# Performance work log

Measured on AMD Instinct MI355X. Metric: run time of the kernel, lower is better.

The kernel has to match this reference:

```python
import jax, jax.numpy as jnp
import numpy as np


def _conv(x, w, b, pad):
    y = jax.lax.conv_general_dilated(x, w, (1, 1), [(pad, pad), (pad, pad)],
                                     dimension_numbers=('NCHW', 'OIHW', 'NCHW'))
    return y + b[None, :, None, None]


def _pool(x):
    return jax.lax.reduce_window(x, -jnp.inf, jax.lax.max, (1, 1, 2, 2), (1, 1, 2, 2), 'VALID')


def _up(x):
    return jnp.repeat(jnp.repeat(x, 2, axis=2), 2, axis=3)


def _unet(x, p):
    r = jax.nn.relu
    e1 = r(_conv(x, p['enc1_w'], p['enc1_b'], 1))                            # [B,16,H,W]
    e2 = r(_conv(_pool(e1), p['enc2_w'], p['enc2_b'], 1))                    # [B,32,H/2,W/2]
    bt = r(_conv(_pool(e2), p['bott_w'], p['bott_b'], 1))                    # [B,64,H/4,W/4]
    d2 = r(_conv(jnp.concatenate([_up(bt), e2], 1), p['dec2_w'], p['dec2_b'], 1))
    d1 = r(_conv(jnp.concatenate([_up(d2), e1], 1), p['dec1_w'], p['dec1_b'], 1))
    return _conv(d1, p['out_w'], p['out_b'], 0)                              # [B,C,H,W]


def _global_match(ref_e, cur_e):
    # FEELVOS global matching: for each current-frame pixel, distance to the
    # nearest reference-frame pixel in embedding space, mapped through
    # d = 1 - 2/(1+exp(||e_p - e_q||^2)). Monotone, so apply after the min.
    N, E, H, W = ref_e.shape
    a = ref_e.reshape(N, E, H * W).transpose(0, 2, 1)   # [N, P, E] reference pixels
    b = cur_e.reshape(N, E, H * W).transpose(0, 2, 1)   # [N, Q, E] current pixels
    d2 = (jnp.sum(a * a, -1)[:, :, None] + jnp.sum(b * b, -1)[:, None, :]
          - 2.0 * jnp.einsum('npe,nqe->npq', a, b))     # [N, P, Q]
    dmin = jnp.min(jnp.maximum(d2, 0.0), axis=1)        # [N, Q] nearest-neighbor dist^2
    return (1.0 - 2.0 * jax.nn.sigmoid(-dmin)).reshape(N, 1, H, W)


def setup_inputs() -> dict:
    key = jax.random.key(0)
    ks = jax.random.split(key, 16)
    B, C, H, W, CIN = 2, 4, 48, 48, 3

    def w(k, shape):
        fan_in = int(np.prod(shape[1:]))
        return jax.random.normal(k, shape, jnp.float32) * np.float32(1.0 / np.sqrt(fan_in))

    return {
        'x1': jax.random.uniform(ks[0], (B, C, H, W), jnp.float32),
        'x2': jax.random.uniform(ks[1], (B, C, H, W), jnp.float32),
        'x3': jax.random.normal(ks[2], (B, CIN, H, W), jnp.float32),
        'enc1_w': w(ks[3], (16, CIN, 3, 3)), 'enc1_b': jnp.zeros((16,), jnp.float32),
        'enc2_w': w(ks[4], (32, 16, 3, 3)), 'enc2_b': jnp.zeros((32,), jnp.float32),
        'bott_w': w(ks[5], (64, 32, 3, 3)), 'bott_b': jnp.zeros((64,), jnp.float32),
        'dec2_w': w(ks[6], (32, 96, 3, 3)), 'dec2_b': jnp.zeros((32,), jnp.float32),
        'dec1_w': w(ks[7], (16, 48, 3, 3)), 'dec1_b': jnp.zeros((16,), jnp.float32),
        'out_w': w(ks[8], (C, 16, 1, 1)), 'out_b': jnp.zeros((C,), jnp.float32),
        'emb_w': w(ks[9], (100, 1, 3, 3)), 'emb_b': jnp.zeros((100,), jnp.float32),
        'dsh_w': w(ks[10], (1, C + 3, 3, 3)), 'dsh_b': jnp.zeros((1,), jnp.float32),
    }


def reference(x1, x2, x3, enc1_w, enc1_b, enc2_w, enc2_b, bott_w, bott_b,
              dec2_w, dec2_b, dec1_w, dec1_b, out_w, out_b, emb_w, emb_b,
              dsh_w, dsh_b):
    p = dict(enc1_w=enc1_w, enc1_b=enc1_b, enc2_w=enc2_w, enc2_b=enc2_b,
             bott_w=bott_w, bott_b=bott_b, dec2_w=dec2_w, dec2_b=dec2_b,
             dec1_w=dec1_w, dec1_b=dec1_b, out_w=out_w, out_b=out_b)
    B, C, H, W = x1.shape
    x3s = _unet(x3, p)                        # backbone on current frame -> [B,C,H,W]
    # fold the per-class Python loop into the batch axis (shared weights)
    x1f = x1.reshape(B * C, 1, H, W)
    x2f = x2.reshape(B * C, 1, H, W)
    x3f = x3s.reshape(B * C, 1, H, W)
    e1 = _conv(x1f, emb_w, emb_b, 1)          # [B*C,100,H,W]
    e2 = _conv(x2f, emb_w, emb_b, 1)
    e3 = _conv(x3f, emb_w, emb_b, 1)
    gm = _global_match(e1, e3)                # first-frame matching  [B*C,1,H,W]
    lm = _global_match(e2, e3)                # previous-frame matching
    x3rep = jnp.broadcast_to(x3s[:, None], (B, C, C, H, W)).reshape(B * C, C, H, W)
    x_t = jnp.concatenate([x3rep, gm, lm, x2f], axis=1)   # [B*C, C+3, H, W]
    logits = _conv(x_t, dsh_w, dsh_b, 1).reshape(B, C, H, W)
    # faithful to the original final loop: output is cat(logits[C-2], logits[C-1])
    return jnp.concatenate([logits[:, C - 2:C - 1], logits[:, C - 1:C]], axis=1)
```

## Files before the change

kernel.cpp:

```cpp
#include <hip/hip_runtime.h>
#include <math.h>

#define THREADS 256
#define HW 2304

typedef __attribute__((ext_vector_type(8))) short short8;
typedef __attribute__((ext_vector_type(4))) float f32x4;
typedef __attribute__((ext_vector_type(8))) unsigned short us8;

typedef const __attribute__((address_space(1))) void* gas_p;
typedef __attribute__((address_space(3))) void* las_p;

__device__ __forceinline__ void gll16(const void* g, const void* l) {
    __builtin_amdgcn_global_load_lds((gas_p)g, (las_p)l, 16, 0, 0);
}

__device__ __forceinline__ void stage_rows(const float* __restrict__ src, float* __restrict__ dst,
                                           int nch, int chStride, int H, int W,
                                           int rlo, int rcount, int tid, int nthr, bool relu) {
    int rowfl = W + 4;
    int total = nch * rcount * rowfl;
    float4 z = make_float4(0.f, 0.f, 0.f, 0.f);
    for (int i = tid; i * 4 < total; i += nthr) ((float4*)dst)[i] = z;
    __syncthreads();
    int w2 = W >> 1;
    int m = nch * rcount * w2;
    for (int i = tid; i < m; i += nthr) {
        int c2 = i % w2;
        int rr = (i / w2) % rcount;
        int ch = i / (w2 * rcount);
        int srow = rlo + rr;
        if (srow < 0 || srow >= H) continue;
        float2 v = *(const float2*)(src + (size_t)ch * chStride + srow * W + 2 * c2);
        if (relu) { v.x = fmaxf(v.x, 0.f); v.y = fmaxf(v.y, 0.f); }
        *(float2*)(dst + (size_t)ch * rcount * rowfl + rr * rowfl + 2 + 2 * c2) = v;
    }
    __syncthreads();
}

#define LOAD_W9(wlbase, ci)                                        \
    const float4* wp4 = (const float4*)((wlbase) + (ci) * 12);     \
    float4 wa = wp4[0], wb = wp4[1], wc = wp4[2];                  \
    const float w9[9] = {wa.x, wa.y, wa.z, wa.w, wb.x, wb.y, wb.z, wb.w, wc.x};

__device__ __forceinline__ void emb_tail(const float* p9, int arr, int ni, int pix,
                                         unsigned short* __restrict__ hl, float* __restrict__ nrm,
                                         const float* wl) {
    float nsum = 0.f;
    char* rowp = (char*)(hl + (((size_t)(arr * 4 + ni)) * HW + pix) * 256);
    for (int g = 0; g < 16; ++g) {
        us8 vh, vl;
        #pragma unroll
        for (int j = 0; j < 8; ++j) {
            int e = g * 8 + j;
            float v = 0.f;
            if (e < 100) {
                v = wl[1200 + e];
                #pragma unroll
                for (int k = 0; k < 9; ++k) v = fmaf(p9[k], wl[e * 12 + k], v);
                nsum = fmaf(v, v, nsum);
            }
            unsigned bits = __float_as_uint(v);
            vh[j] = (unsigned short)(bits >> 16);
            float lo = v - __uint_as_float(bits & 0xFFFF0000u);
            vl[j] = (unsigned short)(__float_as_uint(lo) >> 16);
        }
        *(us8*)(rowp + g * 16) = vh;
        *(us8*)(rowp + 256 + g * 16) = vl;
    }
    nrm[(size_t)(arr * 4 + ni) * HW + pix] = nsum;
}

__device__ __forceinline__ void emb_body(const float* __restrict__ src, int arr, int ni, int pt,
                                         const float* __restrict__ ew, const float* __restrict__ eb,
                                         unsigned short* __restrict__ hl, float* __restrict__ nrm,
                                         float* wl, int tid, int nthr) {
    for (int i = tid; i < 900; i += nthr) wl[(i / 9) * 12 + (i % 9)] = ew[i];
    for (int i = tid; i < 100; i += nthr) wl[1200 + i] = eb[i];
    __syncthreads();

    int pix = pt * 256 + tid;
    int x = pix % 48, y = pix / 48;
    float p9[9];
    #pragma unroll
    for (int ky = 0; ky < 3; ++ky)
        #pragma unroll
        for (int kx = 0; kx < 3; ++kx) {
            int yy = y + ky - 1, xx = x + kx - 1;
            p9[ky * 3 + kx] = (yy >= 0 && yy < 48 && xx >= 0 && xx < 48) ? src[yy * 48 + xx] : 0.f;
        }
    emb_tail(p9, arr, ni, pix, hl, nrm, wl);
}

__global__ __launch_bounds__(256) void k_pre(
        float* __restrict__ d2b, float* __restrict__ d1b,
        const float* __restrict__ b2, const float* __restrict__ b1,
        unsigned* __restrict__ initbuf,
        const float* __restrict__ x3, const float* __restrict__ e1w,
        const float* __restrict__ e1b, float* __restrict__ e1u, float* __restrict__ p1) {
    __shared__ __align__(16) float lds[3 * 50 * 52];
    __shared__ __align__(16) float wl1[48];
    int bx = blockIdx.x;
    int tid = threadIdx.x;
    if (bx < 108) {
        int i4 = bx * 256 + tid;
        if (i4 < 9216) { int ch = (i4 / 144) & 31; float v = b2[ch]; ((float4*)d2b)[i4] = make_float4(v, v, v, v); }
        else { int j = i4 - 9216; int ch = (j / 576) & 15; float v = b1[ch]; ((float4*)d1b)[j] = make_float4(v, v, v, v); }
        return;
    }
    if (bx < 126) {
        int i = (bx - 108) * 256 + tid;
        uint4 f; f.x = f.y = f.z = f.w = 0x7F800000u;
        ((uint4*)initbuf)[i] = f;
        return;
    }
    int co = (bx - 126) & 15, n = (bx - 126) >> 4;
    for (int i = tid; i < 27; i += 256) wl1[(i / 9) * 12 + (i % 9)] = e1w[(co * 3) * 9 + i];
    stage_rows(x3 + (size_t)n * 3 * HW, lds, 3, HW, 48, 48, -1, 50, tid, 256, false);
    float bv = e1b[co];
    for (int o = 0; o < 3; ++o) {
        int po = o * 256 + tid;
        if (po >= 576) break;
        int py = po / 24, px = po % 24;
        float s[2][2] = {{bv, bv}, {bv, bv}};
        for (int ci = 0; ci < 3; ++ci) {
            const float* chp = lds + ci * 2600;
            float c[4][6];
            #pragma unroll
            for (int rr = 0; rr < 4; ++rr) {
                const float2* pr = (const float2*)(chp + (2 * py + rr) * 52);
                #pragma unroll
                for (int k = 0; k < 3; ++k) { float2 t = pr[px + k]; c[rr][2 * k] = t.x; c[rr][2 * k + 1] = t.y; }
            }
            LOAD_W9(wl1, ci)
            #pragma unroll
            for (int dy = 0; dy < 3; ++dy)
                #pragma unroll
                for (int dx = 0; dx < 3; ++dx) {
                    float wv = w9[dy * 3 + dx];
                    #pragma unroll
                    for (int yy = 0; yy < 2; ++yy)
                        #pragma unroll
                        for (int xx = 0; xx < 2; ++xx)
                            s[yy][xx] = fmaf(c[yy + dy][xx + dx + 1], wv, s[yy][xx]);
                }
        }
        float* ob = e1u + (size_t)(n * 16 + co) * HW;
        float mx = -INFINITY;
        #pragma unroll
        for (int yy = 0; yy < 2; ++yy)
            #pragma unroll
            for (int xx = 0; xx < 2; ++xx) {
                float v = fmaxf(s[yy][xx], 0.f);
                ob[(2 * py + yy) * 48 + 2 * px + xx] = v;
                mx = fmaxf(mx, v);
            }
        p1[(size_t)(n * 16 + co) * 576 + py * 24 + px] = mx;
    }
}

__global__ __launch_bounds__(256) void k_enc2pool(const float* __restrict__ p1, const float* __restrict__ w,
                                                  const float* __restrict__ b, float* __restrict__ e2,
                                                  float* __restrict__ p2,
                                                  const float* __restrict__ x1, const float* __restrict__ ew,
                                                  const float* __restrict__ eb,
                                                  unsigned short* __restrict__ hl, float* __restrict__ nrm) {
    __shared__ __align__(16) float smem[11840];
    int tid = threadIdx.x;
    if (blockIdx.x >= 64) {
        int sub = blockIdx.x - 64;
        int ni = sub / 9, pt = sub % 9;
        int plane = 2 + (ni & 1) + 4 * (ni >> 1);
        emb_body(x1 + (size_t)plane * HW, 0, ni, pt, ew, eb, hl, nrm, smem, tid, 256);
        return;
    }
    int co = blockIdx.x & 31, n = blockIdx.x >> 5;
    float* lds = smem;
    float* wl = smem + 11648;
    for (int i = tid; i < 144; i += 256) wl[(i / 9) * 12 + (i % 9)] = w[(co * 16) * 9 + i];
    stage_rows(p1 + (size_t)n * 16 * 576, lds, 16, 576, 24, 24, -1, 26, tid, 256, false);
    if (tid < 144) {
        int py = tid / 12, px = tid % 12;
        float bv = b[co];
        float s[2][2] = {{bv, bv}, {bv, bv}};
        for (int ci = 0; ci < 16; ++ci) {
            const float* chp = lds + ci * 728;
            float c[4][6];
            #pragma unroll
            for (int rr = 0; rr < 4; ++rr) {
                const float2* pr = (const float2*)(chp + (2 * py + rr) * 28);
                #pragma unroll
                for (int k = 0; k < 3; ++k) { float2 t = pr[px + k]; c[rr][2 * k] = t.x; c[rr][2 * k + 1] = t.y; }
            }
            LOAD_W9(wl, ci)
            #pragma unroll
            for (int dy = 0; dy < 3; ++dy)
                #pragma unroll
                for (int dx = 0; dx < 3; ++dx) {
                    float wv = w9[dy * 3 + dx];
                    #pragma unroll
                    for (int yy = 0; yy < 2; ++yy)
                        #pragma unroll
                        for (int xx = 0; xx < 2; ++xx)
                            s[yy][xx] = fmaf(c[yy + dy][xx + dx + 1], wv, s[yy][xx]);
                }
        }
        float* ob = e2 + (size_t)(n * 32 + co) * 576;
        float mx = -INFINITY;
        #pragma unroll
        for (int yy = 0; yy < 2; ++yy)
            #pragma unroll
            for (int xx = 0; xx < 2; ++xx) {
                float v = fmaxf(s[yy][xx], 0.f);
                ob[(2 * py + yy) * 24 + 2 * px + xx] = v;
                mx = fmaxf(mx, v);
            }
        p2[(size_t)(n * 32 + co) * 144 + py * 12 + px] = mx;
    }
}

__global__ __launch_bounds__(256) void k_bott(const float* __restrict__ p2, const float* __restrict__ w,
                                              const float* __restrict__ b, float* __restrict__ bt,
                                              const float* __restrict__ x2, const float* __restrict__ ew,
                                              const float* __restrict__ eb,
                                              unsigned short* __restrict__ hl, float* __restrict__ nrm) {
    __shared__ __align__(16) float smem[7552];
    int tid = threadIdx.x;
    if (blockIdx.x >= 128) {
        int sub = blockIdx.x - 128;
        int ni = sub / 9, pt = sub % 9;
        int plane = 2 + (ni & 1) + 4 * (ni >> 1);
        emb_body(x2 + (size_t)plane * HW, 1, ni, pt, ew, eb, hl, nrm, smem, tid, 256);
        return;
    }
    int co = blockIdx.x & 63, n = blockIdx.x >> 6;
    float* lds = smem;
    float* wl = smem + 7168;
    for (int i = tid; i < 288; i += 256) wl[(i / 9) * 12 + (i % 9)] = w[(co * 32) * 9 + i];
    stage_rows(p2 + (size_t)n * 32 * 144, lds, 32, 144, 12, 12, -1, 14, tid, 256, false);
    if (tid < 144) {
        int y = tid / 12, x = tid % 12;
        float acc = b[co];
        for (int ci = 0; ci < 32; ++ci) {
            const float* chp = lds + ci * 224;
            LOAD_W9(wl, ci)
            #pragma unroll
            for (int dy = 0; dy < 3; ++dy)
                #pragma unroll
                for (int dx = 0; dx < 3; ++dx)
                    acc = fmaf(chp[(y + dy) * 16 + x + dx + 1], w9[dy * 3 + dx], acc);
        }
        bt[(size_t)(n * 64 + co) * 144 + y * 12 + x] = fmaxf(acc, 0.f);
    }
}

__global__ __launch_bounds__(192) void k_dec2p(const float* __restrict__ bt, const float* __restrict__ e2,
                                               const float* __restrict__ w, float* __restrict__ d2b) {
    int bx = blockIdx.x;
    int chunk = bx & 3, co = (bx >> 2) & 31, n = bx >> 7;
    int cib = chunk * 24;
    int nA = max(0, min(24, 64 - cib));
    int nB = 24 - nA;
    int tid = threadIdx.x;
    __shared__ __align__(16) float lds[24 * 26 * 28];
    __shared__ __align__(16) float wl[288];
    for (int i = tid; i < 216; i += 192) wl[(i / 9) * 12 + (i % 9)] = w[((size_t)co * 96 + cib) * 9 + i];
    stage_rows(bt + ((size_t)n * 64 + cib) * 144, lds, nA, 144, 12, 12, -1, 14, tid, 192, false);
    float* ldsB = lds + nA * 224;
    int e2c = max(0, cib + nA - 64);
    stage_rows(e2 + ((size_t)n * 32 + e2c) * 576, ldsB, nB, 576, 24, 24, -1, 26, tid, 192, false);
    if (tid < 144) {
        int y = tid / 6, qx = tid % 6;
        float acc[4] = {0.f, 0.f, 0.f, 0.f};
        int r0 = ((y - 1) >> 1) + 1;
        int yodd = y & 1;
        for (int ci = 0; ci < nA; ++ci) {
            const float* chp = lds + ci * 224;
            const float2* p0 = (const float2*)(chp + r0 * 16);
            const float2* p1 = (const float2*)(chp + (r0 + 1) * 16);
            float a0[6], a1[6], am[6];
            #pragma unroll
            for (int k = 0; k < 3; ++k) {
                float2 t0 = p0[qx + k], t1 = p1[qx + k];
                a0[2 * k] = t0.x; a0[2 * k + 1] = t0.y;
                a1[2 * k] = t1.x; a1[2 * k + 1] = t1.y;
            }
            #pragma unroll
            for (int k = 0; k < 6; ++k) am[k] = yodd ? a0[k] : a1[k];
            LOAD_W9(wl, ci)
            #pragma unroll
            for (int dy = 0; dy < 3; ++dy) {
                const float* rr = (dy == 0) ? a0 : (dy == 1 ? am : a1);
                #pragma unroll
                for (int dx = 0; dx < 3; ++dx) {
                    float wv = w9[dy * 3 + dx];
                    #pragma unroll
                    for (int j = 0; j < 4; ++j)
                        acc[j] = fmaf(rr[((j + dx - 1) >> 1) + 2], wv, acc[j]);
                }
            }
        }
        for (int ci = 0; ci < nB; ++ci) {
            const float* chp = ldsB + ci * 728;
            float bvv[3][8];
            #pragma unroll
            for (int r = 0; r < 3; ++r) {
                const float2* pr = (const float2*)(chp + (y + r) * 28);
                #pragma unroll
                for (int k = 0; k < 4; ++k) { float2 t = pr[2 * qx + k]; bvv[r][2 * k] = t.x; bvv[r][2 * k + 1] = t.y; }
            }
            LOAD_W9(wl, nA + ci)
            #pragma unroll
            for (int dy = 0; dy < 3; ++dy)
                #pragma unroll
                for (int dx = 0; dx < 3; ++dx) {
                    float wv = w9[dy * 3 + dx];
                    #pragma unroll
                    for (int j = 0; j < 4; ++j)
                        acc[j] = fmaf(bvv[dy][j + dx + 1], wv, acc[j]);
                }
        }
        float* op = d2b + ((size_t)(n * 32 + co)) * 576 + y * 24 + qx * 4;
        #pragma unroll
        for (int j = 0; j < 4; ++j) atomicAdd(op + j, acc[j]);
    }
}

__global__ __launch_bounds__(192) void k_dec1p(const float* __restrict__ d2b, const float* __restrict__ e1u,
                                               const float* __restrict__ w, float* __restrict__ d1b) {
    int bx = blockIdx.x;
    int strip = bx % 3;
    int chunk = (bx / 3) & 3;
    int co = (bx / 12) & 15;
    int n = bx / 192;
    int cib = chunk * 12;
    int nA = max(0, min(12, 32 - cib));
    int nB = 12 - nA;
    int y0 = strip * 16;
    int yhlo = (y0 - 1) >> 1;
    int tid = threadIdx.x;
    __shared__ __align__(16) float lds[12 * 18 * 52];
    __shared__ __align__(16) float wl[144];
    for (int i = tid; i < 108; i += 192) wl[(i / 9) * 12 + (i % 9)] = w[((size_t)co * 48 + cib) * 9 + i];
    stage_rows(d2b + ((size_t)n * 32 + cib) * 576, lds, nA, 576, 24, 24, yhlo, 10, tid, 192, true);
    float* ldsB = lds + nA * 280;
    int e1c = max(0, cib + nA - 32);
    stage_rows(e1u + ((size_t)n * 16 + e1c) * HW, ldsB, nB, HW, 48, 48, y0 - 1, 18, tid, 192, false);
    {
        int yl = tid / 12, qx = tid % 12;
        int y = y0 + yl;
        float acc[4] = {0.f, 0.f, 0.f, 0.f};
        int r0 = ((y - 1) >> 1) - yhlo;
        int yodd = y & 1;
        for (int ci = 0; ci < nA; ++ci) {
            const float* chp = lds + ci * 280;
            const float2* p0 = (const float2*)(chp + r0 * 28);
            const float2* p1 = (const float2*)(chp + (r0 + 1) * 28);
            float a0[6], a1[6], am[6];
            #pragma unroll
            for (int k = 0; k < 3; ++k) {
                float2 t0 = p0[qx + k], t1 = p1[qx + k];
                a0[2 * k] = t0.x; a0[2 * k + 1] = t0.y;
                a1[2 * k] = t1.x; a1[2 * k + 1] = t1.y;
            }
            #pragma unroll
            for (int k = 0; k < 6; ++k) am[k] = yodd ? a0[k] : a1[k];
            LOAD_W9(wl, ci)
            #pragma unroll
            for (int dy = 0; dy < 3; ++dy) {
                const float* rr = (dy == 0) ? a0 : (dy == 1 ? am : a1);
                #pragma unroll
                for (int dx = 0; dx < 3; ++dx) {
                    float wv = w9[dy * 3 + dx];
                    #pragma unroll
                    for (int j = 0; j < 4; ++j)
                        acc[j] = fmaf(rr[((j + dx - 1) >> 1) + 2], wv, acc[j]);
                }
            }
        }
        for (int ci = 0; ci < nB; ++ci) {
            const float* chp = ldsB + ci * 936;
            float bvv[3][8];
            #pragma unroll
            for (int r = 0; r < 3; ++r) {
                const float2* pr = (const float2*)(chp + (yl + r) * 52);
                #pragma unroll
                for (int k = 0; k < 4; ++k) { float2 t = pr[2 * qx + k]; bvv[r][2 * k] = t.x; bvv[r][2 * k + 1] = t.y; }
            }
            LOAD_W9(wl, nA + ci)
            #pragma unroll
            for (int dy = 0; dy < 3; ++dy)
                #pragma unroll
                for (int dx = 0; dx < 3; ++dx) {
                    float wv = w9[dy * 3 + dx];
                    #pragma unroll
                    for (int j = 0; j < 4; ++j)
                        acc[j] = fmaf(bvv[dy][j + dx + 1], wv, acc[j]);
                }
        }
        float* op = d1b + ((size_t)(n * 16 + co)) * HW + y * 48 + qx * 4;
        #pragma unroll
        for (int j = 0; j < 4; ++j) atomicAdd(op + j, acc[j]);
    }
}

__global__ __launch_bounds__(256) void k_embout(const float* __restrict__ d1b,
                                                const float* __restrict__ ow, const float* __restrict__ obias,
                                                const float* __restrict__ ew, const float* __restrict__ eb,
                                                unsigned short* __restrict__ hl, float* __restrict__ nrm,
                                                float* __restrict__ x3s) {
    __shared__ float wl[1300];
    int tid = threadIdx.x;
    if (blockIdx.x >= 36) {
        int idx = (blockIdx.x - 36) * 256 + tid;
        int q = idx % HW;
        int co = (idx / HW) & 3;
        int n = idx / 9216;
        float acc = obias[co];
        #pragma unroll
        for (int ci = 0; ci < 16; ++ci)
            acc = fmaf(fmaxf(d1b[((size_t)(n * 16 + ci)) * HW + q], 0.f), ow[co * 16 + ci], acc);
        x3s[((size_t)(n * 4 + co)) * HW + q] = acc;
        return;
    }
    int ni = blockIdx.x / 9, pt = blockIdx.x % 9;
    int n = ni >> 1, co = 2 + (ni & 1);
    for (int i = tid; i < 900; i += 256) wl[(i / 9) * 12 + (i % 9)] = ew[i];
    for (int i = tid; i < 100; i += 256) wl[1200 + i] = eb[i];
    __syncthreads();

    float owr[16];
    #pragma unroll
    for (int k = 0; k < 16; ++k) owr[k] = ow[co * 16 + k];
    float ob = obias[co];
    const float* dp = d1b + (size_t)n * 16 * HW;

    int pix = pt * 256 + tid;
    int x = pix % 48, y = pix / 48;
    float p9[9];
    #pragma unroll
    for (int ky = 0; ky < 3; ++ky)
        #pragma unroll
        for (int kx = 0; kx < 3; ++kx) {
            int yy = y + ky - 1, xx = x + kx - 1;
            float v = 0.f;
            if (yy >= 0 && yy < 48 && xx >= 0 && xx < 48) {
                v = ob;
                int off = yy * 48 + xx;
                #pragma unroll
                for (int ci = 0; ci < 16; ++ci)
                    v = fmaf(fmaxf(dp[(size_t)ci * HW + off], 0.f), owr[ci], v);
            }
            p9[ky * 3 + kx] = v;
        }
    emb_tail(p9, 2, ni, pix, hl, nrm, wl);
}

#define NPC 24
__global__ __launch_bounds__(256, 2) void k_match(
        const unsigned short* __restrict__ hl, const float* __restrict__ nrm,
        unsigned* __restrict__ gmd, unsigned* __restrict__ lmd) {
    int bx = blockIdx.x;
    int l = (bx & 7) * 54 + (bx >> 3);
    int ps = l % 3;
    int qt = (l / 3) % 18;
    int mn = l / 54;
    int n = mn & 3;
    int m = mn >> 2;

    const unsigned short* curhl = hl + ((size_t)(8 + n)) * HW * 256;
    const unsigned short* refhl = hl + ((size_t)(m * 4 + n)) * HW * 256;
    const float* na = nrm + (size_t)(m * 4 + n) * HW;
    const float* nb = nrm + (size_t)(8 + n) * HW;
    unsigned* outd = (m == 0 ? gmd : lmd) + (size_t)n * HW;

    int qbase = qt * 128;
    int pbase = ps * 768;

    __shared__ __align__(16) unsigned short refl[2][32 * 256];
    __shared__ __align__(16) float nal[768];

    int tid = threadIdx.x;
    int wave = tid >> 6;
    int lane = tid & 63;
    int lr = lane >> 5;
    int lc = lane & 31;

    if (tid < 192) *(float4*)&nal[tid * 4] = *(const float4*)(na + pbase + tid * 4);

    short8 ahi[2][4], alo[2][4];
    #pragma unroll
    for (int j = 0; j < 2; ++j) {
        int r = qbase + wave * 32 + j * 16 + (lane & 15);
        const unsigned short* rp = curhl + (size_t)r * 256;
        #pragma unroll
        for (int ks = 0; ks < 4; ++ks) {
            const unsigned short* p = rp + (ks * 4 + (lane >> 4)) * 8;
            ahi[j][ks] = *(const short8*)p;
            alo[j][ks] = *(const short8*)(p + 128);
        }
    }

    {
        const unsigned short* gb = refhl + (size_t)pbase * 256;
        #pragma unroll
        for (int t = 0; t < 4; ++t) {
            int i = wave * 4 + t;
            int r = 2 * i + lr;
            gll16(gb + (size_t)r * 256 + (lc ^ (r & 7)) * 8, &refl[0][i * 512]);
        }
    }
    asm volatile("s_waitcnt lgkmcnt(0)" ::: "memory");

    float dmin[2][4];
    #pragma unroll
    for (int j = 0; j < 2; ++j)
        #pragma unroll
        for (int r = 0; r < 4; ++r) dmin[j][r] = INFINITY;

    for (int pc = 0; pc < NPC; ++pc) {
        int cur = pc & 1;
        if (pc + 1 < NPC) {
            const unsigned short* gb = refhl + (size_t)(pbase + (pc + 1) * 32) * 256;
            #pragma unroll
            for (int t = 0; t < 4; ++t) {
                int i = wave * 4 + t;
                int r = 2 * i + lr;
                gll16(gb + (size_t)r * 256 + (lc ^ (r & 7)) * 8, &refl[cur ^ 1][i * 512]);
            }
            asm volatile("s_waitcnt vmcnt(4)" ::: "memory");
        } else {
            asm volatile("s_waitcnt vmcnt(0)" ::: "memory");
        }
        __builtin_amdgcn_s_barrier();

        short8 bhi[2][4], blo[2][4];
        #pragma unroll
        for (int ptile = 0; ptile < 2; ++ptile) {
            int r = ptile * 16 + (lane & 15);
            #pragma unroll
            for (int ks = 0; ks < 4; ++ks) {
                int cg = ks * 4 + (lane >> 4);
                const char* p = (const char*)refl[cur] + r * 512 + ((cg ^ (r & 7)) << 4);
                bhi[ptile][ks] = *(const short8*)p;
                blo[ptile][ks] = *(const short8*)(p + 256);
            }
        }

        f32x4 acc[2][2];
        #pragma unroll
        for (int ptile = 0; ptile < 2; ++ptile)
            #pragma unroll
            for (int j = 0; j < 2; ++j) acc[ptile][j] = (f32x4){0.f, 0.f, 0.f, 0.f};

        #pragma unroll
        for (int ks = 0; ks < 4; ++ks) {
            #pragma unroll
            for (int ptile = 0; ptile < 2; ++ptile)
                #pragma unroll
                for (int j = 0; j < 2; ++j)
                    acc[ptile][j] = __builtin_amdgcn_mfma_f32_16x16x32_bf16(
                        ahi[j][ks], bhi[ptile][ks], acc[ptile][j], 0, 0, 0);
            #pragma unroll
            for (int ptile = 0; ptile < 2; ++ptile)
                #pragma unroll
                for (int j = 0; j < 2; ++j)
                    acc[ptile][j] = __builtin_amdgcn_mfma_f32_16x16x32_bf16(
                        ahi[j][ks], blo[ptile][ks], acc[ptile][j], 0, 0, 0);
            #pragma unroll
            for (int ptile = 0; ptile < 2; ++ptile)
                #pragma unroll
                for (int j = 0; j < 2; ++j)
                    acc[ptile][j] = __builtin_amdgcn_mfma_f32_16x16x32_bf16(
                        alo[j][ks], bhi[ptile][ks], acc[ptile][j], 0, 0, 0);
        }

        #pragma unroll
        for (int ptile = 0; ptile < 2; ++ptile) {
            float nav = nal[pc * 32 + ptile * 16 + (lane & 15)];
            #pragma unroll
            for (int j = 0; j < 2; ++j)
                #pragma unroll
                for (int r = 0; r < 4; ++r)
                    dmin[j][r] = fminf(dmin[j][r], fmaf(-2.f, acc[ptile][j][r], nav));
        }
        __builtin_amdgcn_s_barrier();
    }

    #pragma unroll
    for (int j = 0; j < 2; ++j)
        #pragma unroll
        for (int r = 0; r < 4; ++r) {
            float v = dmin[j][r];
            v = fminf(v, __shfl_xor(v, 1, 64));
            v = fminf(v, __shfl_xor(v, 2, 64));
            v = fminf(v, __shfl_xor(v, 4, 64));
            v = fminf(v, __shfl_xor(v, 8, 64));
            if ((lane & 15) == 0) {
                int q = qbase + wave * 32 + j * 16 + 4 * (lane >> 4) + r;
                float d2 = fmaxf(v + nb[q], 0.f);
                atomicMin(&outd[q], __float_as_uint(d2));
            }
        }
}

__global__ void k_final(const float* __restrict__ x3s, const unsigned* __restrict__ gmd,
                        const unsigned* __restrict__ lmd, const float* __restrict__ x2,
                        const float* __restrict__ dshw, const float* __restrict__ dshb,
                        float* __restrict__ out) {
    int idx = blockIdx.x * THREADS + threadIdx.x;
    if (idx >= 9216) return;
    int q = idx % HW, ni = idx / HW;
    int n = 2 + (ni & 1) + 4 * (ni >> 1);
    int b = ni >> 1;
    int x = q % 48, y = q / 48;
    float acc = dshb[0];
    for (int c = 0; c < 7; ++c) {
        const float* wp = dshw + c * 9;
        #pragma unroll
        for (int ky = 0; ky < 3; ++ky) {
            int yy = y + ky - 1;
            if (yy < 0 || yy >= 48) continue;
            #pragma unroll
            for (int kx = 0; kx < 3; ++kx) {
                int xx = x + kx - 1;
                if (xx < 0 || xx >= 48) continue;
                float v;
                if (c < 4) v = x3s[(size_t)(b * 4 + c) * HW + yy * 48 + xx];
                else if (c == 4) {
                    float d2 = __uint_as_float(gmd[(size_t)ni * HW + yy * 48 + xx]);
                    v = 1.f - 2.f / (1.f + expf(d2));
                } else if (c == 5) {
                    float d2 = __uint_as_float(lmd[(size_t)ni * HW + yy * 48 + xx]);
                    v = 1.f - 2.f / (1.f + expf(d2));
                } else v = x2[(size_t)n * HW + yy * 48 + xx];
                acc = fmaf(v, wp[ky * 3 + kx], acc);
            }
        }
    }
    out[idx] = acc;
}

extern "C" void kernel_launch(void* const* d_in, const int* in_sizes, int n_in,
                              void* d_out, int out_size, void* d_ws, size_t ws_size,
                              hipStream_t stream) {
    const float* x1     = (const float*)d_in[0];
    const float* x2     = (const float*)d_in[1];
    const float* x3     = (const float*)d_in[2];
    const float* enc1_w = (const float*)d_in[3];
    const float* enc1_b = (const float*)d_in[4];
    const float* enc2_w = (const float*)d_in[5];
    const float* enc2_b = (const float*)d_in[6];
    const float* bott_w = (const float*)d_in[7];
    const float* bott_b = (const float*)d_in[8];
    const float* dec2_w = (const float*)d_in[9];
    const float* dec2_b = (const float*)d_in[10];
    const float* dec1_w = (const float*)d_in[11];
    const float* dec1_b = (const float*)d_in[12];
    const float* out_w  = (const float*)d_in[13];
    const float* out_b  = (const float*)d_in[14];
    const float* emb_w  = (const float*)d_in[15];
    const float* emb_b  = (const float*)d_in[16];
    const float* dsh_w  = (const float*)d_in[17];
    const float* dsh_b  = (const float*)d_in[18];

    float* w = (float*)d_ws;
    float* e1u  = w;
    float* p1   = w + 73728;
    float* e2   = w + 92160;
    float* p2   = w + 129024;
    float* bt   = w + 138240;
    float* d2b  = w + 156672;
    float* d1b  = w + 193536;
    float* x3s  = w + 267264;
    float* nrm  = w + 285696;
    unsigned* gmd = (unsigned*)(w + 313344);
    unsigned* lmd = (unsigned*)(w + 322560);
    unsigned short* hl = (unsigned short*)(w + 331776);

    k_pre<<<dim3(158), dim3(256), 0, stream>>>(d2b, d1b, dec2_b, dec1_b, gmd,
                                               x3, enc1_w, enc1_b, e1u, p1);
    k_enc2pool<<<dim3(100), dim3(256), 0, stream>>>(p1, enc2_w, enc2_b, e2, p2,
                                                    x1, emb_w, emb_b, hl, nrm);
    k_bott<<<dim3(164), dim3(256), 0, stream>>>(p2, bott_w, bott_b, bt,
                                                x2, emb_w, emb_b, hl, nrm);
    k_dec2p<<<dim3(256), dim3(192), 0, stream>>>(bt, e2, dec2_w, d2b);
    k_dec1p<<<dim3(384), dim3(192), 0, stream>>>(d2b, e1u, dec1_w, d1b);
    k_embout<<<dim3(108), dim3(256), 0, stream>>>(d1b, out_w, out_b, emb_w, emb_b, hl, nrm, x3s);
    k_match<<<dim3(432), dim3(256), 0, stream>>>(hl, nrm, gmd, lmd);
    k_final<<<dim3(36), dim3(THREADS), 0, stream>>>(x3s, gmd, lmd, x2, dsh_w, dsh_b, (float*)d_out);
}
```

Baseline: 139.2 us.

## Enlarge match tiles to 192x1152 and stage embout input rows in LDS

```diff
diff --git a/kernel.cpp b/kernel.cpp
--- a/kernel.cpp
+++ b/kernel.cpp
@@ -410,6 +410,7 @@
                                                 unsigned short* __restrict__ hl, float* __restrict__ nrm,
                                                 float* __restrict__ x3s) {
     __shared__ float wl[1300];
+    __shared__ __align__(16) float dl[16][8][48];
     int tid = threadIdx.x;
     if (blockIdx.x >= 36) {
         int idx = (blockIdx.x - 36) * 256 + tid;
@@ -427,13 +428,29 @@
     int n = ni >> 1, co = 2 + (ni & 1);
     for (int i = tid; i < 900; i += 256) wl[(i / 9) * 12 + (i % 9)] = ew[i];
     for (int i = tid; i < 100; i += 256) wl[1200 + i] = eb[i];
+
+    int y0 = (pt * 256) / 48;
+    int ylo = y0 - 1;
+    const float* dp = d1b + (size_t)n * 16 * HW;
+    for (int i = tid; i < 1536; i += 256) {
+        int ci = i / 96;
+        int rem = i % 96;
+        int rr = rem / 12, c4 = rem % 12;
+        int yy = ylo + rr;
+        float4 v = make_float4(0.f, 0.f, 0.f, 0.f);
+        if (yy >= 0 && yy < 48) {
+            v = *(const float4*)(dp + (size_t)ci * HW + yy * 48 + c4 * 4);
+            v.x = fmaxf(v.x, 0.f); v.y = fmaxf(v.y, 0.f);
+            v.z = fmaxf(v.z, 0.f); v.w = fmaxf(v.w, 0.f);
+        }
+        *(float4*)&dl[ci][rr][c4 * 4] = v;
+    }
     __syncthreads();
 
     float owr[16];
     #pragma unroll
     for (int k = 0; k < 16; ++k) owr[k] = ow[co * 16 + k];
     float ob = obias[co];
-    const float* dp = d1b + (size_t)n * 16 * HW;
 
     int pix = pt * 256 + tid;
     int x = pix % 48, y = pix / 48;
@@ -446,25 +463,25 @@
             float v = 0.f;
             if (yy >= 0 && yy < 48 && xx >= 0 && xx < 48) {
                 v = ob;
-                int off = yy * 48 + xx;
+                int rr = yy - ylo;
                 #pragma unroll
                 for (int ci = 0; ci < 16; ++ci)
-                    v = fmaf(fmaxf(dp[(size_t)ci * HW + off], 0.f), owr[ci], v);
+                    v = fmaf(dl[ci][rr][xx], owr[ci], v);
             }
             p9[ky * 3 + kx] = v;
         }
     emb_tail(p9, 2, ni, pix, hl, nrm, wl);
 }
 
-#define NPC 24
-__global__ __launch_bounds__(256, 2) void k_match(
+#define NPC 36
+__global__ __launch_bounds__(256) void k_match(
         const unsigned short* __restrict__ hl, const float* __restrict__ nrm,
         unsigned* __restrict__ gmd, unsigned* __restrict__ lmd) {
     int bx = blockIdx.x;
-    int l = (bx & 7) * 54 + (bx >> 3);
-    int ps = l % 3;
-    int qt = (l / 3) % 18;
-    int mn = l / 54;
+    int mn = bx & 7;
+    int rest = bx >> 3;
+    int qt = rest % 12;
+    int ps = rest / 12;
     int n = mn & 3;
     int m = mn >> 2;
 
@@ -474,11 +491,11 @@
     const float* nb = nrm + (size_t)(8 + n) * HW;
     unsigned* outd = (m == 0 ? gmd : lmd) + (size_t)n * HW;
 
-    int qbase = qt * 128;
-    int pbase = ps * 768;
+    int qbase = qt * 192;
+    int pbase = ps * 1152;
 
     __shared__ __align__(16) unsigned short refl[2][32 * 256];
-    __shared__ __align__(16) float nal[768];
+    __shared__ __align__(16) float nal[1152];
 
     int tid = threadIdx.x;
     int wave = tid >> 6;
@@ -486,12 +503,13 @@
     int lr = lane >> 5;
     int lc = lane & 31;
 
-    if (tid < 192) *(float4*)&nal[tid * 4] = *(const float4*)(na + pbase + tid * 4);
-
-    short8 ahi[2][4], alo[2][4];
+    for (int i = tid; i < 288; i += 256)
+        *(float4*)&nal[i * 4] = *(const float4*)(na + pbase + i * 4);
+
+    short8 ahi[3][4], alo[3][4];
     #pragma unroll
-    for (int j = 0; j < 2; ++j) {
-        int r = qbase + wave * 32 + j * 16 + (lane & 15);
+    for (int j = 0; j < 3; ++j) {
+        int r = qbase + wave * 48 + j * 16 + (lane & 15);
         const unsigned short* rp = curhl + (size_t)r * 256;
         #pragma unroll
         for (int ks = 0; ks < 4; ++ks) {
@@ -512,9 +530,9 @@
     }
     asm volatile("s_waitcnt lgkmcnt(0)" ::: "memory");
 
-    float dmin[2][4];
+    float dmin[3][4];
     #pragma unroll
-    for (int j = 0; j < 2; ++j)
+    for (int j = 0; j < 3; ++j)
         #pragma unroll
         for (int r = 0; r < 4; ++r) dmin[j][r] = INFINITY;
 
@@ -534,52 +552,48 @@
         }
         __builtin_amdgcn_s_barrier();
 
-        short8 bhi[2][4], blo[2][4];
-        #pragma unroll
-        for (int ptile = 0; ptile < 2; ++ptile) {
-            int r = ptile * 16 + (lane & 15);
-            #pragma unroll
-            for (int ks = 0; ks < 4; ++ks) {
-                int cg = ks * 4 + (lane >> 4);
+        f32x4 acc[2][3];
+        #pragma unroll
+        for (int ptile = 0; ptile < 2; ++ptile)
+            #pragma unroll
+            for (int j = 0; j < 3; ++j) acc[ptile][j] = (f32x4){0.f, 0.f, 0.f, 0.f};
+
+        #pragma unroll
+        for (int ks = 0; ks < 4; ++ks) {
+            short8 bhi[2], blo[2];
+            int cg = ks * 4 + (lane >> 4);
+            #pragma unroll
+            for (int ptile = 0; ptile < 2; ++ptile) {
+                int r = ptile * 16 + (lane & 15);
                 const char* p = (const char*)refl[cur] + r * 512 + ((cg ^ (r & 7)) << 4);
-                bhi[ptile][ks] = *(const short8*)p;
-                blo[ptile][ks] = *(const short8*)(p + 256);
-            }
-        }
-
-        f32x4 acc[2][2];
-        #pragma unroll
-        for (int ptile = 0; ptile < 2; ++ptile)
-            #pragma unroll
-            for (int j = 0; j < 2; ++j) acc[ptile][j] = (f32x4){0.f, 0.f, 0.f, 0.f};
-
-        #pragma unroll
-        for (int ks = 0; ks < 4; ++ks) {
+                bhi[ptile] = *(const short8*)p;
+                blo[ptile] = *(const short8*)(p + 256);
+            }
             #pragma unroll
             for (int ptile = 0; ptile < 2; ++ptile)
                 #pragma unroll
-                for (int j = 0; j < 2; ++j)
+                for (int j = 0; j < 3; ++j)
                     acc[ptile][j] = __builtin_amdgcn_mfma_f32_16x16x32_bf16(
-                        ahi[j][ks], bhi[ptile][ks], acc[ptile][j], 0, 0, 0);
+                        ahi[j][ks], bhi[ptile], acc[ptile][j], 0, 0, 0);
             #pragma unroll
             for (int ptile = 0; ptile < 2; ++ptile)
                 #pragma unroll
-                for (int j = 0; j < 2; ++j)
+                for (int j = 0; j < 3; ++j)
                     acc[ptile][j] = __builtin_amdgcn_mfma_f32_16x16x32_bf16(
-                        ahi[j][ks], blo[ptile][ks], acc[ptile][j], 0, 0, 0);
+                        ahi[j][ks], blo[ptile], acc[ptile][j], 0, 0, 0);
             #pragma unroll
             for (int ptile = 0; ptile < 2; ++ptile)
                 #pragma unroll
-                for (int j = 0; j < 2; ++j)
+                for (int j = 0; j < 3; ++j)
                     acc[ptile][j] = __builtin_amdgcn_mfma_f32_16x16x32_bf16(
-                        alo[j][ks], bhi[ptile][ks], acc[ptile][j], 0, 0, 0);
+                        alo[j][ks], bhi[ptile], acc[ptile][j], 0, 0, 0);
         }
 
         #pragma unroll
         for (int ptile = 0; ptile < 2; ++ptile) {
             float nav = nal[pc * 32 + ptile * 16 + (lane & 15)];
             #pragma unroll
-            for (int j = 0; j < 2; ++j)
+            for (int j = 0; j < 3; ++j)
                 #pragma unroll
                 for (int r = 0; r < 4; ++r)
                     dmin[j][r] = fminf(dmin[j][r], fmaf(-2.f, acc[ptile][j][r], nav));
@@ -588,7 +602,7 @@
     }
 
     #pragma unroll
-    for (int j = 0; j < 2; ++j)
+    for (int j = 0; j < 3; ++j)
         #pragma unroll
         for (int r = 0; r < 4; ++r) {
             float v = dmin[j][r];
@@ -597,7 +611,7 @@
             v = fminf(v, __shfl_xor(v, 4, 64));
             v = fminf(v, __shfl_xor(v, 8, 64));
             if ((lane & 15) == 0) {
-                int q = qbase + wave * 32 + j * 16 + 4 * (lane >> 4) + r;
+                int q = qbase + wave * 48 + j * 16 + 4 * (lane >> 4) + r;
                 float d2 = fmaxf(v + nb[q], 0.f);
                 atomicMin(&outd[q], __float_as_uint(d2));
             }
@@ -687,6 +701,6 @@
     k_dec2p<<<dim3(256), dim3(192), 0, stream>>>(bt, e2, dec2_w, d2b);
     k_dec1p<<<dim3(384), dim3(192), 0, stream>>>(d2b, e1u, dec1_w, d1b);
     k_embout<<<dim3(108), dim3(256), 0, stream>>>(d1b, out_w, out_b, emb_w, emb_b, hl, nrm, x3s);
-    k_match<<<dim3(432), dim3(256), 0, stream>>>(hl, nrm, gmd, lmd);
+    k_match<<<dim3(192), dim3(256), 0, stream>>>(hl, nrm, gmd, lmd);
     k_final<<<dim3(36), dim3(THREADS), 0, stream>>>(x3s, gmd, lmd, x2, dsh_w, dsh_b, (float*)d_out);
 }
```

New measurement: 155.5 us. +11.7%, slower.
